# Kernel tuning notes

Hardware: AMD Instinct MI355X
Metric: run time of the kernel (lower is better)

The kernel has to match this reference:

```python
import jax, jax.numpy as jnp
import numpy as np

EPS = 1e-8

def l2norm(x, axis=-1):
    norm = jnp.sqrt(jnp.sum(x * x, axis=axis, keepdims=True)) + EPS
    return x / norm

def setup_inputs() -> dict:
    key = jax.random.key(0)
    ks = jax.random.split(key, 4)
    B, Lq, Ls, d, sim_dim = 128, 128, 256, 1024, 256
    query = jax.random.normal(ks[0], (B, Lq, d), dtype=jnp.float32)
    context = jax.random.normal(ks[1], (B, Ls, d), dtype=jnp.float32)
    matrix = jax.random.uniform(ks[2], (B, Lq, d), dtype=jnp.float32)
    W = jax.random.normal(ks[3], (sim_dim, d), dtype=jnp.float32) * (1.0 / np.sqrt(d))
    b = jnp.zeros((sim_dim,), dtype=jnp.float32)
    smooth = 9
    return {"query": query, "context": context, "matrix": matrix, "W": W, "b": b, "smooth": smooth}

def reference(query, context, matrix, W, b, smooth):
    # cross_attention
    q = query * matrix                                   # (B, Lq, d)
    attn = jnp.einsum('bsd,bqd->bsq', context, q)        # (B, Ls, Lq)
    attn = jnp.where(attn >= 0, attn, 0.1 * attn)        # LeakyReLU(0.1)
    attn = l2norm(attn, axis=-1)                         # normalize over Lq
    attn = jnp.swapaxes(attn, 1, 2)                      # (B, Lq, Ls)
    attn = jax.nn.softmax(attn * smooth, axis=2)         # softmax over source
    wcontext = jnp.einsum('bqs,bsd->bqd', attn, context) # (B, Lq, d)
    wcontext = l2norm(wcontext, axis=-1)
    # alignment vector
    sim_rep = (query - wcontext) ** 2                    # (B, Lq, d)
    sim_rep = jnp.einsum('bqd,kd->bqk', sim_rep, W) + b  # Linear d -> sim_dim
    sim_rep = l2norm(sim_rep, axis=-1)
    return sim_rep
```

## Files before the change

kernel.cpp:

```cpp
#include <hip/hip_runtime.h>
#include <hip/hip_bf16.h>

constexpr int B  = 128;
constexpr int LQ = 128;
constexpr int LS = 256;
constexpr int D  = 1024;
constexpr int SD = 256;
constexpr float EPS = 1e-8f;

typedef __attribute__((ext_vector_type(8))) __bf16 bf16x8;
typedef __attribute__((ext_vector_type(4))) float f32x4;

__device__ inline ushort f2bf(float f) {
    union { float f; uint u; } v{f};
    uint r = v.u + 0x7fffu + ((v.u >> 16) & 1u);
    return (ushort)(r >> 16);
}
__device__ inline float bf2f(ushort u) {
    union { uint u; float f; } v{(uint)u << 16};
    return v.f;
}
__device__ inline uint4 pack8(float4 a, float4 b) {
    union { ushort us[8]; uint4 u4; } r;
    r.us[0]=f2bf(a.x); r.us[1]=f2bf(a.y); r.us[2]=f2bf(a.z); r.us[3]=f2bf(a.w);
    r.us[4]=f2bf(b.x); r.us[5]=f2bf(b.y); r.us[6]=f2bf(b.z); r.us[7]=f2bf(b.w);
    return r.u4;
}
__device__ inline int swz(int row, int kbyte) {
    return row * 128 + (kbyte ^ ((row & 7) << 4));
}
__device__ inline bf16x8 lds_frag(const ushort* base, int row, int kk, int lane) {
    int kbyte = kk * 64 + (lane >> 4) * 16;
    return *(const bf16x8*)((const char*)base + swz(row, kbyte));
}
__device__ inline int swz512(int row, int kbyte) {
    return row * 512 + (kbyte ^ ((row & 7) << 4));
}
__device__ inline f32x4 mfma16(bf16x8 a, bf16x8 b, f32x4 c) {
    return __builtin_amdgcn_mfma_f32_16x16x32_bf16(a, b, c, 0, 0, 0);
}

__global__ __launch_bounds__(256) void wconv_kernel(
    const float* __restrict__ W, ushort* __restrict__ Wb)
{
    size_t i = ((size_t)blockIdx.x * 256 + threadIdx.x) * 8;
    float4 a = *(const float4*)(W + i);
    float4 b = *(const float4*)(W + i + 4);
    *(uint4*)(Wb + i) = pack8(a, b);
}

__global__ __launch_bounds__(512) void gemmA_kernel(
    const float* __restrict__ query, const float* __restrict__ mat,
    const float* __restrict__ ctx, const int* __restrict__ smooth_p,
    ushort* __restrict__ E)
{
    const int bid = blockIdx.x;
    const int xcd = bid & 7, idx = bid >> 3;
    const int b  = xcd * 16 + (idx >> 2);
    const int n0 = (idx & 3) * 64;
    __shared__ ushort As[2][128 * 64];
    __shared__ ushort Bs[2][64 * 64];
    __shared__ float colssP[2][64];
    __shared__ float invsm[64];
    const int t = threadIdx.x;
    const int wv = t >> 6, l = t & 63;
    const int wq = wv >> 2, wsv = wv & 3;

    const float* Qb = query + (size_t)b * LQ * D;
    const float* Mb = mat   + (size_t)b * LQ * D;
    const float* Cb = ctx   + ((size_t)b * LS + n0) * D;
    const int r0 = t >> 3, k8 = (t & 7) * 8;

    f32x4 acc[4] = {};
    float4 q0, q1, q2, q3, m0, m1, m2, m3, c0, c1;

    {
        const float* qp = Qb + (size_t)r0 * D + k8;
        const float* mp = Mb + (size_t)r0 * D + k8;
        q0 = *(const float4*)qp;  q1 = *(const float4*)(qp + 4);
        m0 = *(const float4*)mp;  m1 = *(const float4*)(mp + 4);
        qp += (size_t)64 * D;  mp += (size_t)64 * D;
        q2 = *(const float4*)qp;  q3 = *(const float4*)(qp + 4);
        m2 = *(const float4*)mp;  m3 = *(const float4*)(mp + 4);
        const float* cp = Cb + (size_t)r0 * D + k8;
        c0 = *(const float4*)cp;  c1 = *(const float4*)(cp + 4);
    }
    {
        float4 p1{q0.x*m0.x, q0.y*m0.y, q0.z*m0.z, q0.w*m0.w};
        float4 p2{q1.x*m1.x, q1.y*m1.y, q1.z*m1.z, q1.w*m1.w};
        *(uint4*)((char*)As[0] + swz(r0, k8 * 2)) = pack8(p1, p2);
        float4 p3{q2.x*m2.x, q2.y*m2.y, q2.z*m2.z, q2.w*m2.w};
        float4 p4{q3.x*m3.x, q3.y*m3.y, q3.z*m3.z, q3.w*m3.w};
        *(uint4*)((char*)As[0] + swz(r0 + 64, k8 * 2)) = pack8(p3, p4);
        *(uint4*)((char*)Bs[0] + swz(r0, k8 * 2)) = pack8(c0, c1);
    }
    __syncthreads();

    int cur = 0;
#pragma unroll 1
    for (int ks = 0; ks < 15; ++ks) {
        const int k0 = (ks + 1) * 64;
        {
            const float* qp = Qb + (size_t)r0 * D + k0 + k8;
            const float* mp = Mb + (size_t)r0 * D + k0 + k8;
            q0 = *(const float4*)qp;  q1 = *(const float4*)(qp + 4);
            m0 = *(const float4*)mp;  m1 = *(const float4*)(mp + 4);
            qp += (size_t)64 * D;  mp += (size_t)64 * D;
            q2 = *(const float4*)qp;  q3 = *(const float4*)(qp + 4);
            m2 = *(const float4*)mp;  m3 = *(const float4*)(mp + 4);
            const float* cp = Cb + (size_t)r0 * D + k0 + k8;
            c0 = *(const float4*)cp;  c1 = *(const float4*)(cp + 4);
        }
#pragma unroll
        for (int kk = 0; kk < 2; ++kk) {
            bf16x8 bfr = lds_frag(Bs[cur], wsv * 16 + (l & 15), kk, l);
#pragma unroll
            for (int i = 0; i < 4; ++i) {
                bf16x8 af = lds_frag(As[cur], wq * 64 + i * 16 + (l & 15), kk, l);
                acc[i] = mfma16(af, bfr, acc[i]);
            }
        }
        {
            float4 p1{q0.x*m0.x, q0.y*m0.y, q0.z*m0.z, q0.w*m0.w};
            float4 p2{q1.x*m1.x, q1.y*m1.y, q1.z*m1.z, q1.w*m1.w};
            *(uint4*)((char*)As[cur ^ 1] + swz(r0, k8 * 2)) = pack8(p1, p2);
            float4 p3{q2.x*m2.x, q2.y*m2.y, q2.z*m2.z, q2.w*m2.w};
            float4 p4{q3.x*m3.x, q3.y*m3.y, q3.z*m3.z, q3.w*m3.w};
            *(uint4*)((char*)As[cur ^ 1] + swz(r0 + 64, k8 * 2)) = pack8(p3, p4);
            *(uint4*)((char*)Bs[cur ^ 1] + swz(r0, k8 * 2)) = pack8(c0, c1);
        }
        __syncthreads();
        cur ^= 1;
    }
#pragma unroll
    for (int kk = 0; kk < 2; ++kk) {
        bf16x8 bfr = lds_frag(Bs[cur], wsv * 16 + (l & 15), kk, l);
#pragma unroll
        for (int i = 0; i < 4; ++i) {
            bf16x8 af = lds_frag(As[cur], wq * 64 + i * 16 + (l & 15), kk, l);
            acc[i] = mfma16(af, bfr, acc[i]);
        }
    }

    float csum = 0.f;
#pragma unroll
    for (int i = 0; i < 4; ++i)
#pragma unroll
        for (int r = 0; r < 4; ++r) {
            float v = acc[i][r];
            v = v >= 0.f ? v : 0.1f * v;
            acc[i][r] = v;
            csum += v * v;
        }
    csum += __shfl_xor(csum, 16);
    csum += __shfl_xor(csum, 32);
    if (l < 16) colssP[wq][wsv * 16 + l] = csum;
    __syncthreads();
    const float sm = (float)(*smooth_p);
    if (t < 64) invsm[t] = sm / (sqrtf(colssP[0][t] + colssP[1][t]) + EPS);
    __syncthreads();
    const float invc = invsm[wsv * 16 + (l & 15)];
    ushort* Eb = E + (size_t)b * LQ * LS + n0 + wsv * 16 + (l & 15);
#pragma unroll
    for (int i = 0; i < 4; ++i)
#pragma unroll
        for (int r = 0; r < 4; ++r) {
            int row = wq * 64 + i * 16 + (l >> 4) * 4 + r;
            Eb[(size_t)row * LS] = f2bf(__expf(acc[i][r] * invc));
        }
}

__global__ __launch_bounds__(512) void pv_kernel(
    const ushort* __restrict__ E, const float* __restrict__ ctx,
    ushort* __restrict__ wctx, float* __restrict__ rowssP)
{
    const int bid = blockIdx.x;
    const int xcd = bid & 7, idx = bid >> 3;
    const int b  = xcd * 16 + (idx >> 1);
    const int dh = idx & 1;
    const int dglob0 = dh * 512;

    __shared__ ushort Es[128 * 256];
    __shared__ ushort Bs[64 * 264];
    __shared__ float rsumL[128];
    __shared__ float rinv[128];
    __shared__ float rowssL[128][4];

    const int t = threadIdx.x;
    const int wv = t >> 6, l = t & 63;
    const int wq = wv >> 2, wd = wv & 3;

    const ushort* Eb = E + (size_t)b * LQ * LS;
    const int cc = t & 31, rr = t >> 5;
    float part[8];
#pragma unroll
    for (int p = 0; p < 8; ++p) {
        int row = rr + p * 16;
        uint4 v = *(const uint4*)(Eb + (size_t)row * LS + cc * 8);
        *(uint4*)((char*)Es + swz512(row, cc * 16)) = v;
        const ushort* us = (const ushort*)&v;
        float s = 0.f;
#pragma unroll
        for (int j = 0; j < 8; ++j) s += bf2f(us[j]);
        part[p] = s;
    }
    rowssL[t >> 2][t & 3] = 0.f;
#pragma unroll
    for (int p = 0; p < 8; ++p) {
        float s = part[p];
        s += __shfl_xor(s, 1);  s += __shfl_xor(s, 2);
        s += __shfl_xor(s, 4);  s += __shfl_xor(s, 8);
        s += __shfl_xor(s, 16);
        if ((l & 31) == 0) rsumL[rr + p * 16] = s;
    }

    const float* Cb = ctx + (size_t)b * LS * D + dglob0;
    const int sr = t >> 4, c4 = (t & 15) * 4;
    float4 cr[8];
#pragma unroll
    for (int p = 0; p < 8; ++p)
        cr[p] = *(const float4*)(Cb + (size_t)(p * 32 + sr) * D + c4);

    __syncthreads();
    if (t < 128) rinv[t] = 1.0f / rsumL[t];

#pragma unroll
    for (int p = 0; p < 8; ++p) {
        int s = p * 32 + sr;
        Bs[(c4 + 0) * 264 + s] = f2bf(cr[p].x);
        Bs[(c4 + 1) * 264 + s] = f2bf(cr[p].y);
        Bs[(c4 + 2) * 264 + s] = f2bf(cr[p].z);
        Bs[(c4 + 3) * 264 + s] = f2bf(cr[p].w);
    }
    __syncthreads();

    ushort* Ob = wctx + (size_t)b * LQ * D + dglob0;

#pragma unroll 1
    for (int dt = 0; dt < 8; ++dt) {
        if (dt < 7) {
#pragma unroll
            for (int p = 0; p < 8; ++p)
                cr[p] = *(const float4*)(Cb + (size_t)(p * 32 + sr) * D + (dt + 1) * 64 + c4);
        }
        f32x4 acc[4] = {};
#pragma unroll
        for (int kk = 0; kk < 8; ++kk) {
            const ushort* bp = Bs + (wd * 16 + (l & 15)) * 264 + kk * 32 + (l >> 4) * 8;
            bf16x8 bfr = *(const bf16x8*)bp;
#pragma unroll
            for (int i = 0; i < 4; ++i) {
                bf16x8 af = *(const bf16x8*)((const char*)Es +
                    swz512(wq * 64 + i * 16 + (l & 15), kk * 64 + (l >> 4) * 16));
                acc[i] = mfma16(af, bfr, acc[i]);
            }
        }
#pragma unroll
        for (int i = 0; i < 4; ++i)
#pragma unroll
            for (int r = 0; r < 4; ++r) {
                int row = wq * 64 + i * 16 + (l >> 4) * 4 + r;
                float wval = acc[i][r] * rinv[row];
                float p2 = wval * wval;
                p2 += __shfl_xor(p2, 1); p2 += __shfl_xor(p2, 2);
                p2 += __shfl_xor(p2, 4); p2 += __shfl_xor(p2, 8);
                if ((l & 15) == 0) rowssL[row][wd] += p2;
                Ob[(size_t)row * D + dt * 64 + wd * 16 + (l & 15)] = f2bf(wval);
            }
        __syncthreads();
        if (dt < 7) {
#pragma unroll
            for (int p = 0; p < 8; ++p) {
                int s = p * 32 + sr;
                Bs[(c4 + 0) * 264 + s] = f2bf(cr[p].x);
                Bs[(c4 + 1) * 264 + s] = f2bf(cr[p].y);
                Bs[(c4 + 2) * 264 + s] = f2bf(cr[p].z);
                Bs[(c4 + 3) * 264 + s] = f2bf(cr[p].w);
            }
            __syncthreads();
        }
    }
    if (t < 128)
        rowssP[(size_t)b * 256 + dh * 128 + t] =
            rowssL[t][0] + rowssL[t][1] + rowssL[t][2] + rowssL[t][3];
}

__global__ __launch_bounds__(512) void gemm3_kernel(
    const ushort* __restrict__ wctx, const float* __restrict__ query,
    const float* __restrict__ rowssP, const ushort* __restrict__ Wb,
    const float* __restrict__ bias, float* __restrict__ out)
{
    const int m0 = blockIdx.x * 64;
    const int b  = blockIdx.y;
    __shared__ ushort As[64 * 64];
    __shared__ ushort Bs[256 * 64];
    __shared__ float red[64][4];
    __shared__ float invr[64];
    const int t = threadIdx.x;
    const int w = t >> 6, l = t & 63;
    const int wm = (w >> 2) * 32, wn = (w & 3) * 64;

    const int arow = t >> 3, ako = (t & 7) * 8;
    const float r0v = rowssP[(size_t)b * 256 + m0 + arow];
    const float r1v = rowssP[(size_t)b * 256 + 128 + m0 + arow];
    const float ivq = 1.0f / (sqrtf(r0v + r1v) + EPS);
    const float* Qp  = query + ((size_t)b * LQ + m0 + arow) * D + ako;
    const ushort* Wp = wctx  + ((size_t)b * LQ + m0 + arow) * D + ako;

    f32x4 acc[2][4] = {};

    for (int k0 = 0; k0 < D; k0 += 64) {
        if (k0) __syncthreads();
        {
            uint4 wu = *(const uint4*)(Wp + k0);
            float4 q1 = *(const float4*)(Qp + k0);
            float4 q2 = *(const float4*)(Qp + k0 + 4);
            float d0 = q1.x - bf2f((ushort)(wu.x & 0xffff)) * ivq;
            float d1 = q1.y - bf2f((ushort)(wu.x >> 16))    * ivq;
            float d2 = q1.z - bf2f((ushort)(wu.y & 0xffff)) * ivq;
            float d3 = q1.w - bf2f((ushort)(wu.y >> 16))    * ivq;
            float d4 = q2.x - bf2f((ushort)(wu.z & 0xffff)) * ivq;
            float d5 = q2.y - bf2f((ushort)(wu.z >> 16))    * ivq;
            float d6 = q2.z - bf2f((ushort)(wu.w & 0xffff)) * ivq;
            float d7 = q2.w - bf2f((ushort)(wu.w >> 16))    * ivq;
            float4 s1{d0*d0, d1*d1, d2*d2, d3*d3};
            float4 s2{d4*d4, d5*d5, d6*d6, d7*d7};
            *(uint4*)((char*)As + swz(arow, ako * 2)) = pack8(s1, s2);
        }
#pragma unroll
        for (int j = 0; j < 4; ++j) {
            int c = t + j * 512;
            int row = c >> 3, ko = (c & 7) * 8;
            *(uint4*)((char*)Bs + swz(row, ko * 2)) =
                *(const uint4*)(Wb + (size_t)row * D + k0 + ko);
        }
        __syncthreads();
#pragma unroll
        for (int kk = 0; kk < 2; ++kk) {
            bf16x8 af[2], bfr[4];
#pragma unroll
            for (int i = 0; i < 2; ++i) af[i] = lds_frag(As, wm + i * 16 + (l & 15), kk, l);
#pragma unroll
            for (int n = 0; n < 4; ++n) bfr[n] = lds_frag(Bs, wn + n * 16 + (l & 15), kk, l);
#pragma unroll
            for (int i = 0; i < 2; ++i)
#pragma unroll
                for (int n = 0; n < 4; ++n) acc[i][n] = mfma16(af[i], bfr[n], acc[i][n]);
        }
    }
#pragma unroll
    for (int n = 0; n < 4; ++n) {
        float bv = bias[wn + n * 16 + (l & 15)];
#pragma unroll
        for (int i = 0; i < 2; ++i)
#pragma unroll
            for (int r = 0; r < 4; ++r) acc[i][n][r] += bv;
    }
#pragma unroll
    for (int i = 0; i < 2; ++i)
#pragma unroll
        for (int r = 0; r < 4; ++r) {
            float p = 0.f;
#pragma unroll
            for (int n = 0; n < 4; ++n) p += acc[i][n][r] * acc[i][n][r];
#pragma unroll
            for (int off = 1; off < 16; off <<= 1) p += __shfl_xor(p, off);
            int rowl = wm + i * 16 + (l >> 4) * 4 + r;
            if ((l & 15) == 0) red[rowl][w & 3] = p;
        }
    __syncthreads();
    if (t < 64) {
        float s = red[t][0] + red[t][1] + red[t][2] + red[t][3];
        invr[t] = 1.0f / (sqrtf(s) + EPS);
    }
    __syncthreads();
    float* Ob = out + ((size_t)b * LQ + m0) * SD;
#pragma unroll
    for (int i = 0; i < 2; ++i)
#pragma unroll
        for (int r = 0; r < 4; ++r) {
            int rowl = wm + i * 16 + (l >> 4) * 4 + r;
            float iv = invr[rowl];
#pragma unroll
            for (int n = 0; n < 4; ++n) {
                int col = wn + n * 16 + (l & 15);
                Ob[(size_t)rowl * SD + col] = acc[i][n][r] * iv;
            }
        }
}

extern "C" void kernel_launch(void* const* d_in, const int* in_sizes, int n_in,
                              void* d_out, int out_size, void* d_ws, size_t ws_size,
                              hipStream_t stream)
{
    const float* query  = (const float*)d_in[0];
    const float* ctx    = (const float*)d_in[1];
    const float* mat    = (const float*)d_in[2];
    const float* W      = (const float*)d_in[3];
    const float* bias   = (const float*)d_in[4];
    const int*   smooth = (const int*)d_in[5];
    float* out = (float*)d_out;

    char* ws = (char*)d_ws;
    ushort* wctx   = (ushort*)ws;
    ushort* E      = (ushort*)(ws + (size_t)32 * 1024 * 1024);
    ushort* Wb     = (ushort*)(ws + (size_t)40 * 1024 * 1024);
    float*  rowssP = (float*)(ws + (size_t)(40 * 1024 + 512) * 1024);

    wconv_kernel<<<dim3(SD * D / (256 * 8)), 256, 0, stream>>>(W, Wb);
    gemmA_kernel<<<dim3(512), 512, 0, stream>>>(query, mat, ctx, smooth, E);
    pv_kernel<<<dim3(256), 512, 0, stream>>>(E, ctx, wctx, rowssP);
    gemm3_kernel<<<dim3(2, B), 512, 0, stream>>>(wctx, query, rowssP, Wb, bias, out);
}
```

Before: 156.3 us.

## Pre-convert query*matrix and context to bf16 and stage E stores through LDS

Adds two elementwise kernels: one writes query*matrix and the other writes context to bf16 workspace buffers. gemmA and pv then read the half-size bf16 data instead of fp32 and no longer convert inside their loops. gemmA also stages its exp scores in shared memory so the E writes to global memory are coalesced 16-byte stores instead of scattered 2-byte ones. The cost is two extra kernel launches and an extra full read of the fp32 inputs plus a write of the bf16 copies. The wctx buffer reuses the qm region, which is safe only because qm is dead after gemmA.

```diff
diff --git a/kernel.cpp b/kernel.cpp
--- a/kernel.cpp
+++ b/kernel.cpp
@@ -49,10 +49,30 @@
     *(uint4*)(Wb + i) = pack8(a, b);
 }
 
+__global__ __launch_bounds__(256) void qmconv_kernel(
+    const float* __restrict__ query, const float* __restrict__ mat,
+    ushort* __restrict__ qm)
+{
+    size_t i = ((size_t)blockIdx.x * 256 + threadIdx.x) * 8;
+    float4 q1 = *(const float4*)(query + i), q2 = *(const float4*)(query + i + 4);
+    float4 m1 = *(const float4*)(mat + i),   m2 = *(const float4*)(mat + i + 4);
+    float4 p1{q1.x*m1.x, q1.y*m1.y, q1.z*m1.z, q1.w*m1.w};
+    float4 p2{q2.x*m2.x, q2.y*m2.y, q2.z*m2.z, q2.w*m2.w};
+    *(uint4*)(qm + i) = pack8(p1, p2);
+}
+
+__global__ __launch_bounds__(256) void cconv_kernel(
+    const float* __restrict__ ctx, ushort* __restrict__ ctxB)
+{
+    size_t i = ((size_t)blockIdx.x * 256 + threadIdx.x) * 8;
+    float4 a = *(const float4*)(ctx + i);
+    float4 b = *(const float4*)(ctx + i + 4);
+    *(uint4*)(ctxB + i) = pack8(a, b);
+}
+
 __global__ __launch_bounds__(512) void gemmA_kernel(
-    const float* __restrict__ query, const float* __restrict__ mat,
-    const float* __restrict__ ctx, const int* __restrict__ smooth_p,
-    ushort* __restrict__ E)
+    const ushort* __restrict__ qm, const ushort* __restrict__ ctxB,
+    const int* __restrict__ smooth_p, ushort* __restrict__ E)
 {
     const int bid = blockIdx.x;
     const int xcd = bid & 7, idx = bid >> 3;
@@ -62,55 +82,33 @@
     __shared__ ushort Bs[2][64 * 64];
     __shared__ float colssP[2][64];
     __shared__ float invsm[64];
+    ushort* Et = (ushort*)As;
     const int t = threadIdx.x;
     const int wv = t >> 6, l = t & 63;
     const int wq = wv >> 2, wsv = wv & 3;
 
-    const float* Qb = query + (size_t)b * LQ * D;
-    const float* Mb = mat   + (size_t)b * LQ * D;
-    const float* Cb = ctx   + ((size_t)b * LS + n0) * D;
+    const ushort* Ab = qm   + (size_t)b * LQ * D;
+    const ushort* Cb = ctxB + ((size_t)b * LS + n0) * D;
     const int r0 = t >> 3, k8 = (t & 7) * 8;
 
     f32x4 acc[4] = {};
-    float4 q0, q1, q2, q3, m0, m1, m2, m3, c0, c1;
-
-    {
-        const float* qp = Qb + (size_t)r0 * D + k8;
-        const float* mp = Mb + (size_t)r0 * D + k8;
-        q0 = *(const float4*)qp;  q1 = *(const float4*)(qp + 4);
-        m0 = *(const float4*)mp;  m1 = *(const float4*)(mp + 4);
-        qp += (size_t)64 * D;  mp += (size_t)64 * D;
-        q2 = *(const float4*)qp;  q3 = *(const float4*)(qp + 4);
-        m2 = *(const float4*)mp;  m3 = *(const float4*)(mp + 4);
-        const float* cp = Cb + (size_t)r0 * D + k8;
-        c0 = *(const float4*)cp;  c1 = *(const float4*)(cp + 4);
-    }
-    {
-        float4 p1{q0.x*m0.x, q0.y*m0.y, q0.z*m0.z, q0.w*m0.w};
-        float4 p2{q1.x*m1.x, q1.y*m1.y, q1.z*m1.z, q1.w*m1.w};
-        *(uint4*)((char*)As[0] + swz(r0, k8 * 2)) = pack8(p1, p2);
-        float4 p3{q2.x*m2.x, q2.y*m2.y, q2.z*m2.z, q2.w*m2.w};
-        float4 p4{q3.x*m3.x, q3.y*m3.y, q3.z*m3.z, q3.w*m3.w};
-        *(uint4*)((char*)As[0] + swz(r0 + 64, k8 * 2)) = pack8(p3, p4);
-        *(uint4*)((char*)Bs[0] + swz(r0, k8 * 2)) = pack8(c0, c1);
-    }
+    uint4 a0, a1, b0;
+
+    a0 = *(const uint4*)(Ab + (size_t)r0 * D + k8);
+    a1 = *(const uint4*)(Ab + (size_t)(r0 + 64) * D + k8);
+    b0 = *(const uint4*)(Cb + (size_t)r0 * D + k8);
+    *(uint4*)((char*)As[0] + swz(r0, k8 * 2))      = a0;
+    *(uint4*)((char*)As[0] + swz(r0 + 64, k8 * 2)) = a1;
+    *(uint4*)((char*)Bs[0] + swz(r0, k8 * 2))      = b0;
     __syncthreads();
 
     int cur = 0;
 #pragma unroll 1
     for (int ks = 0; ks < 15; ++ks) {
         const int k0 = (ks + 1) * 64;
-        {
-            const float* qp = Qb + (size_t)r0 * D + k0 + k8;
-            const float* mp = Mb + (size_t)r0 * D + k0 + k8;
-            q0 = *(const float4*)qp;  q1 = *(const float4*)(qp + 4);
-            m0 = *(const float4*)mp;  m1 = *(const float4*)(mp + 4);
-            qp += (size_t)64 * D;  mp += (size_t)64 * D;
-            q2 = *(const float4*)qp;  q3 = *(const float4*)(qp + 4);
-            m2 = *(const float4*)mp;  m3 = *(const float4*)(mp + 4);
-            const float* cp = Cb + (size_t)r0 * D + k0 + k8;
-            c0 = *(const float4*)cp;  c1 = *(const float4*)(cp + 4);
-        }
+        a0 = *(const uint4*)(Ab + (size_t)r0 * D + k0 + k8);
+        a1 = *(const uint4*)(Ab + (size_t)(r0 + 64) * D + k0 + k8);
+        b0 = *(const uint4*)(Cb + (size_t)r0 * D + k0 + k8);
 #pragma unroll
         for (int kk = 0; kk < 2; ++kk) {
             bf16x8 bfr = lds_frag(Bs[cur], wsv * 16 + (l & 15), kk, l);
@@ -120,15 +118,9 @@
                 acc[i] = mfma16(af, bfr, acc[i]);
             }
         }
-        {
-            float4 p1{q0.x*m0.x, q0.y*m0.y, q0.z*m0.z, q0.w*m0.w};
-            float4 p2{q1.x*m1.x, q1.y*m1.y, q1.z*m1.z, q1.w*m1.w};
-            *(uint4*)((char*)As[cur ^ 1] + swz(r0, k8 * 2)) = pack8(p1, p2);
-            float4 p3{q2.x*m2.x, q2.y*m2.y, q2.z*m2.z, q2.w*m2.w};
-            float4 p4{q3.x*m3.x, q3.y*m3.y, q3.z*m3.z, q3.w*m3.w};
-            *(uint4*)((char*)As[cur ^ 1] + swz(r0 + 64, k8 * 2)) = pack8(p3, p4);
-            *(uint4*)((char*)Bs[cur ^ 1] + swz(r0, k8 * 2)) = pack8(c0, c1);
-        }
+        *(uint4*)((char*)As[cur ^ 1] + swz(r0, k8 * 2))      = a0;
+        *(uint4*)((char*)As[cur ^ 1] + swz(r0 + 64, k8 * 2)) = a1;
+        *(uint4*)((char*)Bs[cur ^ 1] + swz(r0, k8 * 2))      = b0;
         __syncthreads();
         cur ^= 1;
     }
@@ -160,18 +152,25 @@
     if (t < 64) invsm[t] = sm / (sqrtf(colssP[0][t] + colssP[1][t]) + EPS);
     __syncthreads();
     const float invc = invsm[wsv * 16 + (l & 15)];
-    ushort* Eb = E + (size_t)b * LQ * LS + n0 + wsv * 16 + (l & 15);
 #pragma unroll
     for (int i = 0; i < 4; ++i)
 #pragma unroll
         for (int r = 0; r < 4; ++r) {
             int row = wq * 64 + i * 16 + (l >> 4) * 4 + r;
-            Eb[(size_t)row * LS] = f2bf(__expf(acc[i][r] * invc));
-        }
+            Et[row * 72 + wsv * 16 + (l & 15)] = f2bf(__expf(acc[i][r] * invc));
+        }
+    __syncthreads();
+    ushort* Eg = E + (size_t)b * LQ * LS + n0;
+#pragma unroll
+    for (int j = 0; j < 2; ++j) {
+        int c = t + j * 512;
+        int row = c >> 3, s8 = (c & 7) * 8;
+        *(uint4*)(Eg + (size_t)row * LS + s8) = *(const uint4*)(Et + row * 72 + s8);
+    }
 }
 
 __global__ __launch_bounds__(512) void pv_kernel(
-    const ushort* __restrict__ E, const float* __restrict__ ctx,
+    const ushort* __restrict__ E, const ushort* __restrict__ ctxB,
     ushort* __restrict__ wctx, float* __restrict__ rowssP)
 {
     const int bid = blockIdx.x;
@@ -214,12 +213,12 @@
         if ((l & 31) == 0) rsumL[rr + p * 16] = s;
     }
 
-    const float* Cb = ctx + (size_t)b * LS * D + dglob0;
+    const ushort* Cb = ctxB + (size_t)b * LS * D + dglob0;
     const int sr = t >> 4, c4 = (t & 15) * 4;
-    float4 cr[8];
+    uint2 cr[8];
 #pragma unroll
     for (int p = 0; p < 8; ++p)
-        cr[p] = *(const float4*)(Cb + (size_t)(p * 32 + sr) * D + c4);
+        cr[p] = *(const uint2*)(Cb + (size_t)(p * 32 + sr) * D + c4);
 
     __syncthreads();
     if (t < 128) rinv[t] = 1.0f / rsumL[t];
@@ -227,10 +226,11 @@
 #pragma unroll
     for (int p = 0; p < 8; ++p) {
         int s = p * 32 + sr;
-        Bs[(c4 + 0) * 264 + s] = f2bf(cr[p].x);
-        Bs[(c4 + 1) * 264 + s] = f2bf(cr[p].y);
-        Bs[(c4 + 2) * 264 + s] = f2bf(cr[p].z);
-        Bs[(c4 + 3) * 264 + s] = f2bf(cr[p].w);
+        const ushort* us = (const ushort*)&cr[p];
+        Bs[(c4 + 0) * 264 + s] = us[0];
+        Bs[(c4 + 1) * 264 + s] = us[1];
+        Bs[(c4 + 2) * 264 + s] = us[2];
+        Bs[(c4 + 3) * 264 + s] = us[3];
     }
     __syncthreads();
 
@@ -241,7 +241,7 @@
         if (dt < 7) {
 #pragma unroll
             for (int p = 0; p < 8; ++p)
-                cr[p] = *(const float4*)(Cb + (size_t)(p * 32 + sr) * D + (dt + 1) * 64 + c4);
+                cr[p] = *(const uint2*)(Cb + (size_t)(p * 32 + sr) * D + (dt + 1) * 64 + c4);
         }
         f32x4 acc[4] = {};
 #pragma unroll
@@ -272,10 +272,11 @@
 #pragma unroll
             for (int p = 0; p < 8; ++p) {
                 int s = p * 32 + sr;
-                Bs[(c4 + 0) * 264 + s] = f2bf(cr[p].x);
-                Bs[(c4 + 1) * 264 + s] = f2bf(cr[p].y);
-                Bs[(c4 + 2) * 264 + s] = f2bf(cr[p].z);
-                Bs[(c4 + 3) * 264 + s] = f2bf(cr[p].w);
+                const ushort* us = (const ushort*)&cr[p];
+                Bs[(c4 + 0) * 264 + s] = us[0];
+                Bs[(c4 + 1) * 264 + s] = us[1];
+                Bs[(c4 + 2) * 264 + s] = us[2];
+                Bs[(c4 + 3) * 264 + s] = us[3];
             }
             __syncthreads();
         }
@@ -402,13 +403,17 @@
     float* out = (float*)d_out;
 
     char* ws = (char*)d_ws;
-    ushort* wctx   = (ushort*)ws;
-    ushort* E      = (ushort*)(ws + (size_t)32 * 1024 * 1024);
-    ushort* Wb     = (ushort*)(ws + (size_t)40 * 1024 * 1024);
-    float*  rowssP = (float*)(ws + (size_t)(40 * 1024 + 512) * 1024);
+    ushort* ctxB   = (ushort*)ws;
+    ushort* qm     = (ushort*)(ws + (size_t)64 * 1024 * 1024);
+    ushort* wctx   = qm;
+    ushort* E      = (ushort*)(ws + (size_t)96 * 1024 * 1024);
+    ushort* Wb     = (ushort*)(ws + (size_t)104 * 1024 * 1024);
+    float*  rowssP = (float*)(ws + (size_t)(104 * 1024 + 512) * 1024);
 
     wconv_kernel<<<dim3(SD * D / (256 * 8)), 256, 0, stream>>>(W, Wb);
-    gemmA_kernel<<<dim3(512), 512, 0, stream>>>(query, mat, ctx, smooth, E);
-    pv_kernel<<<dim3(256), 512, 0, stream>>>(E, ctx, wctx, rowssP);
+    qmconv_kernel<<<dim3((size_t)B * LQ * D / (256 * 8)), 256, 0, stream>>>(query, mat, qm);
+    cconv_kernel<<<dim3((size_t)B * LS * D / (256 * 8)), 256, 0, stream>>>(ctx, ctxB);
+    gemmA_kernel<<<dim3(512), 512, 0, stream>>>(qm, ctxB, smooth, E);
+    pv_kernel<<<dim3(256), 512, 0, stream>>>(E, ctxB, wctx, rowssP);
     gemm3_kernel<<<dim3(2, B), 512, 0, stream>>>(wctx, query, rowssP, Wb, bias, out);
 }
```

New measurement: 177.6 us. +13.6%, slower.

## Widen gemmA tile to 128 source columns and stage output through LDS

Applied to the files above, without the earlier changes.

Each gemmA block now covers 128 context rows instead of 64, so the query*matrix A tile is loaded and converted once per two column blocks. This halves redundant global reads of query and matrix and halves the grid to 256 blocks. The exp'd scores are staged in shared memory and written back with coalesced 16-byte stores instead of scattered 2-byte stores. In exchange, each thread holds twice as many accumulators, there is less block-level parallelism, and the kernel uses more LDS.

```diff
diff --git a/kernel.cpp b/kernel.cpp
--- a/kernel.cpp
+++ b/kernel.cpp
@@ -56,12 +56,13 @@
 {
     const int bid = blockIdx.x;
     const int xcd = bid & 7, idx = bid >> 3;
-    const int b  = xcd * 16 + (idx >> 2);
-    const int n0 = (idx & 3) * 64;
-    __shared__ ushort As[2][128 * 64];
-    __shared__ ushort Bs[2][64 * 64];
-    __shared__ float colssP[2][64];
-    __shared__ float invsm[64];
+    const int b  = xcd * 16 + (idx >> 1);
+    const int n0 = (idx & 1) * 128;
+    __shared__ ushort SH[4][128 * 64];
+    __shared__ float colssP[2][128];
+    __shared__ float invsm[128];
+    ushort* Et = &SH[0][0];
+
     const int t = threadIdx.x;
     const int wv = t >> 6, l = t & 63;
     const int wq = wv >> 2, wsv = wv & 3;
@@ -71,103 +72,100 @@
     const float* Cb = ctx   + ((size_t)b * LS + n0) * D;
     const int r0 = t >> 3, k8 = (t & 7) * 8;
 
-    f32x4 acc[4] = {};
-    float4 q0, q1, q2, q3, m0, m1, m2, m3, c0, c1;
-
-    {
-        const float* qp = Qb + (size_t)r0 * D + k8;
-        const float* mp = Mb + (size_t)r0 * D + k8;
-        q0 = *(const float4*)qp;  q1 = *(const float4*)(qp + 4);
-        m0 = *(const float4*)mp;  m1 = *(const float4*)(mp + 4);
+    f32x4 acc[4][2] = {};
+    float4 q0,q1,q2,q3, m0,m1,m2,m3, c0,c1,c2,c3;
+
+    auto loadT = [&](int k0) {
+        const float* qp = Qb + (size_t)r0 * D + k0 + k8;
+        const float* mp = Mb + (size_t)r0 * D + k0 + k8;
+        q0 = *(const float4*)qp; q1 = *(const float4*)(qp + 4);
+        m0 = *(const float4*)mp; m1 = *(const float4*)(mp + 4);
         qp += (size_t)64 * D;  mp += (size_t)64 * D;
-        q2 = *(const float4*)qp;  q3 = *(const float4*)(qp + 4);
-        m2 = *(const float4*)mp;  m3 = *(const float4*)(mp + 4);
-        const float* cp = Cb + (size_t)r0 * D + k8;
-        c0 = *(const float4*)cp;  c1 = *(const float4*)(cp + 4);
-    }
-    {
+        q2 = *(const float4*)qp; q3 = *(const float4*)(qp + 4);
+        m2 = *(const float4*)mp; m3 = *(const float4*)(mp + 4);
+        const float* cp = Cb + (size_t)r0 * D + k0 + k8;
+        c0 = *(const float4*)cp; c1 = *(const float4*)(cp + 4);
+        cp += (size_t)64 * D;
+        c2 = *(const float4*)cp; c3 = *(const float4*)(cp + 4);
+    };
+    auto storeT = [&](int buf) {
         float4 p1{q0.x*m0.x, q0.y*m0.y, q0.z*m0.z, q0.w*m0.w};
         float4 p2{q1.x*m1.x, q1.y*m1.y, q1.z*m1.z, q1.w*m1.w};
-        *(uint4*)((char*)As[0] + swz(r0, k8 * 2)) = pack8(p1, p2);
+        *(uint4*)((char*)&SH[buf][0] + swz(r0, k8 * 2)) = pack8(p1, p2);
         float4 p3{q2.x*m2.x, q2.y*m2.y, q2.z*m2.z, q2.w*m2.w};
         float4 p4{q3.x*m3.x, q3.y*m3.y, q3.z*m3.z, q3.w*m3.w};
-        *(uint4*)((char*)As[0] + swz(r0 + 64, k8 * 2)) = pack8(p3, p4);
-        *(uint4*)((char*)Bs[0] + swz(r0, k8 * 2)) = pack8(c0, c1);
-    }
-    __syncthreads();
-
+        *(uint4*)((char*)&SH[buf][0] + swz(r0 + 64, k8 * 2)) = pack8(p3, p4);
+        *(uint4*)((char*)&SH[2 + buf][0] + swz(r0, k8 * 2))      = pack8(c0, c1);
+        *(uint4*)((char*)&SH[2 + buf][0] + swz(r0 + 64, k8 * 2)) = pack8(c2, c3);
+    };
+    auto mfmaT = [&](int buf) {
+#pragma unroll
+        for (int kk = 0; kk < 2; ++kk) {
+            bf16x8 bfr0 = lds_frag(&SH[2 + buf][0], wsv * 32 + (l & 15), kk, l);
+            bf16x8 bfr1 = lds_frag(&SH[2 + buf][0], wsv * 32 + 16 + (l & 15), kk, l);
+#pragma unroll
+            for (int i = 0; i < 4; ++i) {
+                bf16x8 af = lds_frag(&SH[buf][0], wq * 64 + i * 16 + (l & 15), kk, l);
+                acc[i][0] = mfma16(af, bfr0, acc[i][0]);
+                acc[i][1] = mfma16(af, bfr1, acc[i][1]);
+            }
+        }
+    };
+
+    loadT(0);
+    storeT(0);
+    __syncthreads();
     int cur = 0;
 #pragma unroll 1
     for (int ks = 0; ks < 15; ++ks) {
-        const int k0 = (ks + 1) * 64;
-        {
-            const float* qp = Qb + (size_t)r0 * D + k0 + k8;
-            const float* mp = Mb + (size_t)r0 * D + k0 + k8;
-            q0 = *(const float4*)qp;  q1 = *(const float4*)(qp + 4);
-            m0 = *(const float4*)mp;  m1 = *(const float4*)(mp + 4);
-            qp += (size_t)64 * D;  mp += (size_t)64 * D;
-            q2 = *(const float4*)qp;  q3 = *(const float4*)(qp + 4);
-            m2 = *(const float4*)mp;  m3 = *(const float4*)(mp + 4);
-            const float* cp = Cb + (size_t)r0 * D + k0 + k8;
-            c0 = *(const float4*)cp;  c1 = *(const float4*)(cp + 4);
-        }
-#pragma unroll
-        for (int kk = 0; kk < 2; ++kk) {
-            bf16x8 bfr = lds_frag(Bs[cur], wsv * 16 + (l & 15), kk, l);
-#pragma unroll
-            for (int i = 0; i < 4; ++i) {
-                bf16x8 af = lds_frag(As[cur], wq * 64 + i * 16 + (l & 15), kk, l);
-                acc[i] = mfma16(af, bfr, acc[i]);
-            }
-        }
-        {
-            float4 p1{q0.x*m0.x, q0.y*m0.y, q0.z*m0.z, q0.w*m0.w};
-            float4 p2{q1.x*m1.x, q1.y*m1.y, q1.z*m1.z, q1.w*m1.w};
-            *(uint4*)((char*)As[cur ^ 1] + swz(r0, k8 * 2)) = pack8(p1, p2);
-            float4 p3{q2.x*m2.x, q2.y*m2.y, q2.z*m2.z, q2.w*m2.w};
-            float4 p4{q3.x*m3.x, q3.y*m3.y, q3.z*m3.z, q3.w*m3.w};
-            *(uint4*)((char*)As[cur ^ 1] + swz(r0 + 64, k8 * 2)) = pack8(p3, p4);
-            *(uint4*)((char*)Bs[cur ^ 1] + swz(r0, k8 * 2)) = pack8(c0, c1);
-        }
+        loadT((ks + 1) * 64);
+        mfmaT(cur);
+        storeT(cur ^ 1);
         __syncthreads();
         cur ^= 1;
     }
-#pragma unroll
-    for (int kk = 0; kk < 2; ++kk) {
-        bf16x8 bfr = lds_frag(Bs[cur], wsv * 16 + (l & 15), kk, l);
-#pragma unroll
-        for (int i = 0; i < 4; ++i) {
-            bf16x8 af = lds_frag(As[cur], wq * 64 + i * 16 + (l & 15), kk, l);
-            acc[i] = mfma16(af, bfr, acc[i]);
-        }
-    }
-
-    float csum = 0.f;
-#pragma unroll
-    for (int i = 0; i < 4; ++i)
-#pragma unroll
-        for (int r = 0; r < 4; ++r) {
-            float v = acc[i][r];
-            v = v >= 0.f ? v : 0.1f * v;
-            acc[i][r] = v;
-            csum += v * v;
-        }
-    csum += __shfl_xor(csum, 16);
-    csum += __shfl_xor(csum, 32);
-    if (l < 16) colssP[wq][wsv * 16 + l] = csum;
+    mfmaT(cur);
+
+#pragma unroll
+    for (int n = 0; n < 2; ++n) {
+        float csum = 0.f;
+#pragma unroll
+        for (int i = 0; i < 4; ++i)
+#pragma unroll
+            for (int r = 0; r < 4; ++r) {
+                float v = acc[i][n][r];
+                v = v >= 0.f ? v : 0.1f * v;
+                acc[i][n][r] = v;
+                csum += v * v;
+            }
+        csum += __shfl_xor(csum, 16);
+        csum += __shfl_xor(csum, 32);
+        if (l < 16) colssP[wq][wsv * 32 + n * 16 + l] = csum;
+    }
     __syncthreads();
     const float sm = (float)(*smooth_p);
-    if (t < 64) invsm[t] = sm / (sqrtf(colssP[0][t] + colssP[1][t]) + EPS);
-    __syncthreads();
-    const float invc = invsm[wsv * 16 + (l & 15)];
-    ushort* Eb = E + (size_t)b * LQ * LS + n0 + wsv * 16 + (l & 15);
-#pragma unroll
-    for (int i = 0; i < 4; ++i)
-#pragma unroll
-        for (int r = 0; r < 4; ++r) {
-            int row = wq * 64 + i * 16 + (l >> 4) * 4 + r;
-            Eb[(size_t)row * LS] = f2bf(__expf(acc[i][r] * invc));
-        }
+    if (t < 128) invsm[t] = sm / (sqrtf(colssP[0][t] + colssP[1][t]) + EPS);
+    __syncthreads();
+#pragma unroll
+    for (int n = 0; n < 2; ++n) {
+        const float invc = invsm[wsv * 32 + n * 16 + (l & 15)];
+#pragma unroll
+        for (int i = 0; i < 4; ++i)
+#pragma unroll
+            for (int r = 0; r < 4; ++r) {
+                int row = wq * 64 + i * 16 + (l >> 4) * 4 + r;
+                Et[row * 136 + wsv * 32 + n * 16 + (l & 15)] =
+                    f2bf(__expf(acc[i][n][r] * invc));
+            }
+    }
+    __syncthreads();
+    ushort* Eg = E + (size_t)b * LQ * LS + n0;
+#pragma unroll
+    for (int j = 0; j < 4; ++j) {
+        int c = t + j * 512;
+        int row = c >> 4, s8 = (c & 15) * 8;
+        *(uint4*)(Eg + (size_t)row * LS + s8) = *(const uint4*)(Et + row * 136 + s8);
+    }
 }
 
 __global__ __launch_bounds__(512) void pv_kernel(
@@ -408,7 +406,7 @@
     float*  rowssP = (float*)(ws + (size_t)(40 * 1024 + 512) * 1024);
 
     wconv_kernel<<<dim3(SD * D / (256 * 8)), 256, 0, stream>>>(W, Wb);
-    gemmA_kernel<<<dim3(512), 512, 0, stream>>>(query, mat, ctx, smooth, E);
+    gemmA_kernel<<<dim3(256), 512, 0, stream>>>(query, mat, ctx, smooth, E);
     pv_kernel<<<dim3(256), 512, 0, stream>>>(E, ctx, wctx, rowssP);
     gemm3_kernel<<<dim3(2, B), 512, 0, stream>>>(wctx, query, rowssP, Wb, bias, out);
 }
```

New measurement: 150.2 us. -3.9%, faster.
